# Optimization experiments

Measured on AMD Instinct MI355X. Metric: run time of the kernel, lower is better.

Reference implementation:

```python
import jax, jax.numpy as jnp
import numpy as np
import math

B, L, HID = 2, 2048, 1024
NH, DH = 16, 64
MASK_VAL = -1000000000.0  # half_precision_flag == False


def setup_inputs() -> dict:
    key = jax.random.key(0)
    ks = jax.random.split(key, 12)
    s = 0.02
    return {
        "queries": jax.random.normal(ks[0], (B, L, HID), jnp.float32),
        "keys": jax.random.normal(ks[1], (B, L, HID), jnp.float32),
        "values": jax.random.normal(ks[2], (B, L, HID), jnp.float32),
        "mask": jax.random.randint(ks[3], (B, L, L), 0, 2, jnp.int32),
        "Wq": jax.random.normal(ks[4], (HID, NH * DH), jnp.float32) * s,
        "bq": jnp.zeros((NH * DH,), jnp.float32),
        "Wk": jax.random.normal(ks[5], (HID, NH * DH), jnp.float32) * s,
        "bk": jnp.zeros((NH * DH,), jnp.float32),
        "Wv": jax.random.normal(ks[6], (HID, NH * DH), jnp.float32) * s,
        "bv": jnp.zeros((NH * DH,), jnp.float32),
        "Wo": jax.random.normal(ks[7], (NH * DH, HID), jnp.float32) * s,
        "bo": jnp.zeros((HID,), jnp.float32),
    }


def reference(queries, keys, values, mask, Wq, bq, Wk, bk, Wv, bv, Wo, bo):
    # Linear projections: (B, L, NH*DH)
    q = queries @ Wq + bq
    k = keys @ Wk + bk
    v = values @ Wv + bv
    # FAITHFUL to original: raw .view(B, NH, -1, DH) without transpose
    q = q.reshape(B, NH, L, DH)
    k = k.reshape(B, NH, L, DH)
    v = v.reshape(B, NH, L, DH)
    # scaled dot-product scores: (B, NH, L, L)
    scores = jnp.einsum("bhqd,bhkd->bhqk", q, k) / math.sqrt(DH)
    scores = jnp.where(mask[:, None, :, :] == 0, MASK_VAL, scores)
    probs = jax.nn.softmax(scores, axis=-1)  # dropout p=0 -> identity
    ctx = jnp.einsum("bhqk,bhkd->bhqd", probs, v)  # (B, NH, L, DH)
    # transpose(1,2) then flatten heads, as in original
    ctx = ctx.transpose(0, 2, 1, 3).reshape(B, L, NH * DH)
    return ctx @ Wo + bo
```

## Files before the change

kernel.cpp:

```cpp
#include <hip/hip_runtime.h>
#include <stdint.h>

typedef __bf16 bf16;
typedef __bf16 bf16x8 __attribute__((ext_vector_type(8)));
typedef __bf16 bf16x4 __attribute__((ext_vector_type(4)));
typedef float  f32x4  __attribute__((ext_vector_type(4)));
typedef short  s16x4  __attribute__((ext_vector_type(4)));
typedef unsigned long long ull;

#define GLOAD16(gptr, lptr)                                                     \
  __builtin_amdgcn_global_load_lds(                                             \
      (const __attribute__((address_space(1))) void*)(gptr),                    \
      (__attribute__((address_space(3))) void*)(lptr), 16, 0, 0)

#define MFMA16(a, b, c) __builtin_amdgcn_mfma_f32_16x16x32_bf16((a), (b), (c), 0, 0, 0)
#define MFMA16K16(a, b, c) __builtin_amdgcn_mfma_f32_16x16x16bf16_1k((a), (b), (c), 0, 0, 0)

static constexpr int B_ = 2, L_ = 2048, NH_ = 16, DH_ = 64;
static constexpr float QSCALE = 0.18033688011112042f;

__global__ __launch_bounds__(256) void k_prep(const float* __restrict__ q,
                                              const float* __restrict__ k,
                                              const float* __restrict__ v,
                                              const int* __restrict__ mask,
                                              const float* __restrict__ wq,
                                              const float* __restrict__ wk,
                                              const float* __restrict__ wv,
                                              const float* __restrict__ wo,
                                              bf16* __restrict__ X,
                                              bf16* __restrict__ Wt,
                                              ull* __restrict__ mb) {
  __shared__ float t[32][33];
  const int bid = blockIdx.x, tid = threadIdx.x;
  if (bid < 32768) {
    int tt = bid * 256 + tid;
    ull bal = __ballot(mask[tt] != 0);
    if ((tid & 63) == 0) mb[tt >> 6] = bal;
  } else if (bid < 45056) {
    int u = bid - 32768;
    int z = u >> 12, x = u & 4095;
    const float* in = z == 0 ? q : (z == 1 ? k : v);
    bf16* out = X + (size_t)z * 4194304;
    int i = x * 256 + tid;
    const float4 f = ((const float4*)in)[i];
    bf16x4 o = {(bf16)f.x, (bf16)f.y, (bf16)f.z, (bf16)f.w};
    ((bf16x4*)out)[i] = o;
  } else {
    int u = bid - 45056;
    int z = u >> 10, rem = u & 1023;
    const float* in = z == 0 ? wq : (z == 1 ? wk : (z == 2 ? wv : wo));
    bf16* out = Wt + (size_t)z * 1048576;
    int bx = (rem & 31) * 32, by = (rem >> 5) * 32;
    int x = tid & 31, y = tid >> 5;
#pragma unroll
    for (int r = 0; r < 4; ++r)
      t[y + r * 8][x] = in[(size_t)(by + y + r * 8) * 1024 + bx + x];
    __syncthreads();
#pragma unroll
    for (int r = 0; r < 4; ++r)
      out[(size_t)(bx + y + r * 8) * 1024 + by + x] = (bf16)t[x][y + r * 8];
  }
}

__global__ __launch_bounds__(256) void k_gemm3(const bf16* __restrict__ Xb,
                                               const bf16* __restrict__ Wb,
                                               const float* __restrict__ b0,
                                               const float* __restrict__ b1,
                                               const float* __restrict__ b2,
                                               bf16* __restrict__ Ob) {
  const int z = blockIdx.z;
  const bf16* A  = Xb + (size_t)z * 4194304;
  const bf16* Bt = Wb + (size_t)z * 1048576;
  const float* bias = z == 0 ? b0 : (z == 1 ? b1 : b2);
  bf16* C = Ob + (size_t)z * 4194304;
  const int m0 = blockIdx.y * 128, n0 = blockIdx.x * 128;
  __shared__ __align__(16) bf16 As[128 * 32];
  __shared__ __align__(16) bf16 Bs[128 * 32];
  const int tid = threadIdx.x, lane = tid & 63, w = tid >> 6, quad = lane >> 4, l15 = lane & 15;
  const int wm = (w & 1) * 64, wn = (w >> 1) * 64;
  f32x4 acc[4][4] = {};
  for (int kt = 0; kt < 32; ++kt) {
    const int kk = kt * 32;
#pragma unroll
    for (int i = 0; i < 2; ++i) {
      int s = tid + i * 256;
      int r = s >> 2, c = (s & 3) ^ ((r >> 1) & 3);
      GLOAD16(A + (size_t)(m0 + r) * 1024 + kk + c * 8, As + s * 8);
      GLOAD16(Bt + (size_t)(n0 + r) * 1024 + kk + c * 8, Bs + s * 8);
    }
    __syncthreads();
    bf16x8 af[4], bb[4];
#pragma unroll
    for (int i = 0; i < 4; ++i) {
      int ra = wm + i * 16 + l15, rb = wn + i * 16 + l15;
      af[i] = *(const bf16x8*)(As + (ra * 4 + (quad ^ ((ra >> 1) & 3))) * 8);
      bb[i] = *(const bf16x8*)(Bs + (rb * 4 + (quad ^ ((rb >> 1) & 3))) * 8);
    }
#pragma unroll
    for (int mi = 0; mi < 4; ++mi)
#pragma unroll
      for (int ni = 0; ni < 4; ++ni)
        acc[mi][ni] = MFMA16(af[mi], bb[ni], acc[mi][ni]);
    __syncthreads();
  }
  const float scale = (z == 0) ? QSCALE : 1.0f;
#pragma unroll
  for (int mi = 0; mi < 4; ++mi)
#pragma unroll
    for (int ni = 0; ni < 4; ++ni) {
      int row = m0 + wm + mi * 16 + quad * 4;
      int col = n0 + wn + ni * 16 + l15;
      float bz = bias[col];
      if (z == 2) {
        int b_ = row >> 11, l = row & 2047;
        int hh = l >> 7;
        int i0 = (l & 127) * 16 + (col >> 6);
        int d  = col & 63;
        bf16* dst = C + (size_t)(b_ * 16 + hh) * 131072;
#pragma unroll
        for (int r = 0; r < 4; ++r) {
          int iK = i0 + 16 * r;
          dst[((size_t)(iK >> 2) * 64 + d) * 4 + (iK & 3)] = (bf16)(acc[mi][ni][r] + bz);
        }
      } else {
#pragma unroll
        for (int r = 0; r < 4; ++r)
          C[(size_t)(row + r) * 1024 + col] = (bf16)((acc[mi][ni][r] + bz) * scale);
      }
    }
}

__global__ __launch_bounds__(256) void k_gemmo(const bf16* __restrict__ A,
                                               const bf16* __restrict__ Bt,
                                               const float* __restrict__ bias,
                                               float* __restrict__ C) {
  const int m0 = blockIdx.y * 64, n0 = blockIdx.x * 128;
  __shared__ __align__(16) bf16 As[64 * 32];
  __shared__ __align__(16) bf16 Bs[128 * 32];
  const int tid = threadIdx.x, lane = tid & 63, w = tid >> 6, quad = lane >> 4, l15 = lane & 15;
  const int wn = w * 32;
  f32x4 acc[4][2] = {};
  for (int kt = 0; kt < 32; ++kt) {
    const int kk = kt * 32;
    {
      int r = tid >> 2, c = (tid & 3) ^ ((r >> 1) & 3);
      GLOAD16(A + (size_t)(m0 + r) * 1024 + kk + c * 8, As + tid * 8);
    }
#pragma unroll
    for (int i = 0; i < 2; ++i) {
      int s = tid + i * 256;
      int r = s >> 2, c = (s & 3) ^ ((r >> 1) & 3);
      GLOAD16(Bt + (size_t)(n0 + r) * 1024 + kk + c * 8, Bs + s * 8);
    }
    __syncthreads();
    bf16x8 af[4], bb[2];
#pragma unroll
    for (int i = 0; i < 4; ++i) {
      int ra = i * 16 + l15;
      af[i] = *(const bf16x8*)(As + (ra * 4 + (quad ^ ((ra >> 1) & 3))) * 8);
    }
#pragma unroll
    for (int i = 0; i < 2; ++i) {
      int rb = wn + i * 16 + l15;
      bb[i] = *(const bf16x8*)(Bs + (rb * 4 + (quad ^ ((rb >> 1) & 3))) * 8);
    }
#pragma unroll
    for (int mi = 0; mi < 4; ++mi)
#pragma unroll
      for (int ni = 0; ni < 2; ++ni)
        acc[mi][ni] = MFMA16(af[mi], bb[ni], acc[mi][ni]);
    __syncthreads();
  }
#pragma unroll
  for (int mi = 0; mi < 4; ++mi)
#pragma unroll
    for (int ni = 0; ni < 2; ++ni) {
      int row = m0 + mi * 16 + quad * 4;
      int col = n0 + wn + ni * 16 + l15;
      float bz = bias[col];
#pragma unroll
      for (int r = 0; r < 4; ++r)
        C[(size_t)(row + r) * 1024 + col] = acc[mi][ni][r] + bz;
    }
}

__global__ __launch_bounds__(256) void k_flash(const bf16* __restrict__ Qp,
                                               const bf16* __restrict__ Kp,
                                               const bf16* __restrict__ Vtp,
                                               const ull* __restrict__ mb,
                                               bf16* __restrict__ ctx) {
  const int b = blockIdx.z, h = blockIdx.y, q0 = blockIdx.x * 128;
  const size_t HEAD = 131072;
  const bf16* Q  = Qp  + ((size_t)b * NH_ + h) * HEAD;
  const bf16* K  = Kp  + ((size_t)b * NH_ + h) * HEAD;
  const bf16* Vt = Vtp + ((size_t)b * NH_ + h) * HEAD;
  const ull* mrow = mb + (size_t)b * L_ * 32;

  __shared__ __align__(16) bf16 Ks[2][64 * 64];
  __shared__ __align__(16) bf16 Vs[2][64 * 64];
  __shared__ __align__(16) ull  Ms[2][256];

  const int tid = threadIdx.x, lane = tid & 63, w = tid >> 6, quad = lane >> 4, l15 = lane & 15;

  bf16x8 qf[2][2];
#pragma unroll
  for (int qb = 0; qb < 2; ++qb)
#pragma unroll
    for (int ks = 0; ks < 2; ++ks)
      qf[qb][ks] = *(const bf16x8*)(Q + (size_t)(q0 + w * 32 + qb * 16 + l15) * 64 + ks * 32 + quad * 8);

#pragma unroll
  for (int i = 0; i < 2; ++i) {
    int s = tid + i * 256;
    int key = s >> 3, c = (s & 7) ^ (key & 7);
    GLOAD16(K + (size_t)key * 64 + c * 8, Ks[0] + s * 8);
    GLOAD16(Vt + (size_t)s * 8, Vs[0] + s * 8);
  }
  if (w < 2) {
    int r = w * 64 + lane;
    GLOAD16(mrow + (size_t)(q0 + r) * 32, (bf16*)&Ms[0][0] + r * 8);
  }
  __syncthreads();

  f32x4 accO[2][4] = {};
  f32x4 accL[2] = {};
  const s16x4 onesf = {0x3F80, 0x3F80, 0x3F80, 0x3F80};

  for (int kt = 0; kt < 32; ++kt) {
    const int cur = kt & 1;
    if (kt + 1 < 32) {
      const int nxt = cur ^ 1;
#pragma unroll
      for (int i = 0; i < 2; ++i) {
        int s = tid + i * 256;
        int key = s >> 3, c = (s & 7) ^ (key & 7);
        GLOAD16(K + (size_t)((kt + 1) * 64 + key) * 64 + c * 8, Ks[nxt] + s * 8);
        GLOAD16(Vt + (size_t)(kt + 1) * 4096 + s * 8, Vs[nxt] + s * 8);
      }
      if ((kt & 1) && w < 2) {
        int r = w * 64 + lane;
        GLOAD16(mrow + (size_t)(q0 + r) * 32 + (kt + 1),
                (bf16*)&Ms[((kt + 1) >> 1) & 1][0] + r * 8);
      }
    }

    f32x4 st[4][2] = {};
#pragma unroll
    for (int ks = 0; ks < 2; ++ks)
#pragma unroll
      for (int kb = 0; kb < 4; ++kb) {
        int key = kb * 16 + l15;
        bf16x8 kf = *(const bf16x8*)(Ks[cur] + (key * 8 + ((ks * 4 + quad) ^ (key & 7))) * 8);
        st[kb][0] = MFMA16(kf, qf[0][ks], st[kb][0]);
        st[kb][1] = MFMA16(kf, qf[1][ks], st[kb][1]);
      }

    const ull* Mcur = Ms[(kt >> 1) & 1];
    const ull word0 = Mcur[(w * 32 + l15) * 2 + cur];
    const ull word1 = Mcur[(w * 32 + 16 + l15) * 2 + cur];
    s16x4 pf[4][2];
#pragma unroll
    for (int kb = 0; kb < 4; ++kb)
#pragma unroll
      for (int qb = 0; qb < 2; ++qb) {
        const unsigned nib = (unsigned)((qb ? word1 : word0) >> (kb * 16 + quad * 4)) & 0xFu;
        float p0 = (nib & 1u) ? __builtin_amdgcn_exp2f(st[kb][qb][0]) : 0.f;
        float p1 = (nib & 2u) ? __builtin_amdgcn_exp2f(st[kb][qb][1]) : 0.f;
        float p2 = (nib & 4u) ? __builtin_amdgcn_exp2f(st[kb][qb][2]) : 0.f;
        float p3 = (nib & 8u) ? __builtin_amdgcn_exp2f(st[kb][qb][3]) : 0.f;
        bf16x4 pb = {(bf16)p0, (bf16)p1, (bf16)p2, (bf16)p3};
        pf[kb][qb] = __builtin_bit_cast(s16x4, pb);
      }

#pragma unroll
    for (int kb = 0; kb < 4; ++kb) {
      accL[0] = MFMA16K16(pf[kb][0], onesf, accL[0]);
      accL[1] = MFMA16K16(pf[kb][1], onesf, accL[1]);
    }

#pragma unroll
    for (int kb = 0; kb < 4; ++kb)
#pragma unroll
      for (int db = 0; db < 4; ++db) {
        s16x4 vf = *(const s16x4*)(Vs[cur] + ((size_t)((kb * 4 + quad) * 64 + db * 16 + l15)) * 4);
        accO[0][db] = MFMA16K16(pf[kb][0], vf, accO[0][db]);
        accO[1][db] = MFMA16K16(pf[kb][1], vf, accO[1][db]);
      }
    __syncthreads();
  }

#pragma unroll
  for (int qb = 0; qb < 2; ++qb) {
    float rl[4];
#pragma unroll
    for (int r = 0; r < 4; ++r) rl[r] = 1.0f / accL[qb][r];
#pragma unroll
    for (int db = 0; db < 4; ++db) {
      const int col = h * 64 + db * 16 + l15;
#pragma unroll
      for (int r = 0; r < 4; ++r) {
        const int rowg = q0 + w * 32 + qb * 16 + quad * 4 + r;
        ctx[((size_t)b * L_ + rowg) * 1024 + col] = (bf16)(accO[qb][db][r] * rl[r]);
      }
    }
  }
}

extern "C" void kernel_launch(void* const* d_in, const int* in_sizes, int n_in,
                              void* d_out, int out_size, void* d_ws, size_t ws_size,
                              hipStream_t stream) {
  (void)in_sizes; (void)n_in; (void)out_size; (void)ws_size;
  const float* q    = (const float*)d_in[0];
  const float* k    = (const float*)d_in[1];
  const float* v    = (const float*)d_in[2];
  const int*   mask = (const int*)d_in[3];
  const float* Wq = (const float*)d_in[4];
  const float* bq = (const float*)d_in[5];
  const float* Wk = (const float*)d_in[6];
  const float* bk = (const float*)d_in[7];
  const float* Wv = (const float*)d_in[8];
  const float* bv = (const float*)d_in[9];
  const float* Wo = (const float*)d_in[10];
  const float* bo = (const float*)d_in[11];
  float* out = (float*)d_out;

  char* ws = (char*)d_ws;
  const size_t SX = (size_t)4096 * 1024 * 2;
  const size_t SW = (size_t)1024 * 1024 * 2;
  bf16* X   = (bf16*)(ws);
  bf16* Wt  = (bf16*)(ws + 3 * SX);
  bf16* QKV = (bf16*)(ws + 3 * SX + 4 * SW);
  bf16* Qp  = QKV;
  bf16* Kp  = QKV + 4194304;
  bf16* Vtp = QKV + 2 * 4194304;
  bf16* Ctx = (bf16*)(ws + 6 * SX + 4 * SW);
  ull* mbits = (ull*)(ws + 7 * SX + 4 * SW);

  dim3 blk(256);
  k_prep<<<49152, blk, 0, stream>>>(q, k, v, mask, Wq, Wk, Wv, Wo, X, Wt, mbits);

  k_gemm3<<<dim3(8, 32, 3), blk, 0, stream>>>(X, Wt, bq, bk, bv, QKV);

  k_flash<<<dim3(16, NH_, B_), blk, 0, stream>>>(Qp, Kp, Vtp, mbits, Ctx);

  k_gemmo<<<dim3(8, 64), blk, 0, stream>>>(Ctx, Wt + 3 * 1048576, bo, out);
}
```

Baseline: 273.9 us.

## Split attention key range across two blocks and merge partials in a combine kernel

The flash attention kernel now handles only half of the key tiles per block. The grid grows from 512 to 1024 blocks, which should raise occupancy across the CUs. Each half writes unnormalized fp32 partial outputs and row sums to workspace. A new combine kernel adds the two halves, normalizes them and writes the bf16 context. In exchange there is extra global memory traffic for the fp32 partials, one more kernel launch, and workspace aliasing over the dead X buffer and the region past the mask bits.

```diff
diff --git a/kernel.cpp b/kernel.cpp
--- a/kernel.cpp
+++ b/kernel.cpp
@@ -188,13 +188,21 @@
                                                const bf16* __restrict__ Kp,
                                                const bf16* __restrict__ Vtp,
                                                const ull* __restrict__ mb,
-                                               bf16* __restrict__ ctx) {
-  const int b = blockIdx.z, h = blockIdx.y, q0 = blockIdx.x * 128;
+                                               float* __restrict__ O0,
+                                               float* __restrict__ O1,
+                                               float* __restrict__ L0,
+                                               float* __restrict__ L1) {
+  const int b = blockIdx.z >> 1, half = blockIdx.z & 1;
+  const int h = blockIdx.y, q0 = blockIdx.x * 128;
+  const int kt0 = half * 16, ktend = kt0 + 16;
+  float* __restrict__ Op = half ? O1 : O0;
+  float* __restrict__ Lp = half ? L1 : L0;
   const size_t HEAD = 131072;
   const bf16* Q  = Qp  + ((size_t)b * NH_ + h) * HEAD;
   const bf16* K  = Kp  + ((size_t)b * NH_ + h) * HEAD;
   const bf16* Vt = Vtp + ((size_t)b * NH_ + h) * HEAD;
   const ull* mrow = mb + (size_t)b * L_ * 32;
+  const size_t obase = ((size_t)b * NH_ + h) * L_;
 
   __shared__ __align__(16) bf16 Ks[2][64 * 64];
   __shared__ __align__(16) bf16 Vs[2][64 * 64];
@@ -213,12 +221,12 @@
   for (int i = 0; i < 2; ++i) {
     int s = tid + i * 256;
     int key = s >> 3, c = (s & 7) ^ (key & 7);
-    GLOAD16(K + (size_t)key * 64 + c * 8, Ks[0] + s * 8);
-    GLOAD16(Vt + (size_t)s * 8, Vs[0] + s * 8);
+    GLOAD16(K + (size_t)(kt0 * 64 + key) * 64 + c * 8, Ks[0] + s * 8);
+    GLOAD16(Vt + (size_t)kt0 * 4096 + s * 8, Vs[0] + s * 8);
   }
   if (w < 2) {
     int r = w * 64 + lane;
-    GLOAD16(mrow + (size_t)(q0 + r) * 32, (bf16*)&Ms[0][0] + r * 8);
+    GLOAD16(mrow + (size_t)(q0 + r) * 32 + kt0, (bf16*)&Ms[0][0] + r * 8);
   }
   __syncthreads();
 
@@ -226,9 +234,9 @@
   f32x4 accL[2] = {};
   const s16x4 onesf = {0x3F80, 0x3F80, 0x3F80, 0x3F80};
 
-  for (int kt = 0; kt < 32; ++kt) {
+  for (int kt = kt0; kt < ktend; ++kt) {
     const int cur = kt & 1;
-    if (kt + 1 < 32) {
+    if (kt + 1 < ktend) {
       const int nxt = cur ^ 1;
 #pragma unroll
       for (int i = 0; i < 2; ++i) {
@@ -291,19 +299,42 @@
 
 #pragma unroll
   for (int qb = 0; qb < 2; ++qb) {
-    float rl[4];
-#pragma unroll
-    for (int r = 0; r < 4; ++r) rl[r] = 1.0f / accL[qb][r];
 #pragma unroll
     for (int db = 0; db < 4; ++db) {
-      const int col = h * 64 + db * 16 + l15;
+      const int d = db * 16 + l15;
 #pragma unroll
       for (int r = 0; r < 4; ++r) {
-        const int rowg = q0 + w * 32 + qb * 16 + quad * 4 + r;
-        ctx[((size_t)b * L_ + rowg) * 1024 + col] = (bf16)(accO[qb][db][r] * rl[r]);
-      }
-    }
-  }
+        const int qq = q0 + w * 32 + qb * 16 + quad * 4 + r;
+        Op[(obase + qq) * 64 + d] = accO[qb][db][r];
+      }
+    }
+    if (l15 == 0) {
+#pragma unroll
+      for (int r = 0; r < 4; ++r) {
+        const int qq = q0 + w * 32 + qb * 16 + quad * 4 + r;
+        Lp[obase + qq] = accL[qb][r];
+      }
+    }
+  }
+}
+
+__global__ __launch_bounds__(256) void k_comb(const float* __restrict__ O0,
+                                              const float* __restrict__ O1,
+                                              const float* __restrict__ L0,
+                                              const float* __restrict__ L1,
+                                              bf16* __restrict__ ctx) {
+  const int t = blockIdx.x * 256 + threadIdx.x;
+  const int d4 = t & 15;
+  const int q  = (t >> 4) & 2047;
+  const int bh = t >> 15;
+  const size_t base = (((size_t)bh * 2048 + q) * 64) + d4 * 4;
+  const float4 o0 = *(const float4*)(O0 + base);
+  const float4 o1 = *(const float4*)(O1 + base);
+  const float rl = 1.0f / (L0[(size_t)bh * 2048 + q] + L1[(size_t)bh * 2048 + q]);
+  const int b = bh >> 4, h = bh & 15;
+  bf16x4 r = {(bf16)((o0.x + o1.x) * rl), (bf16)((o0.y + o1.y) * rl),
+              (bf16)((o0.z + o1.z) * rl), (bf16)((o0.w + o1.w) * rl)};
+  *(bf16x4*)(ctx + ((size_t)(b * 2048 + q) * 1024 + h * 64 + d4 * 4)) = r;
 }
 
 extern "C" void kernel_launch(void* const* d_in, const int* in_sizes, int n_in,
@@ -327,6 +358,7 @@
   char* ws = (char*)d_ws;
   const size_t SX = (size_t)4096 * 1024 * 2;
   const size_t SW = (size_t)1024 * 1024 * 2;
+  const size_t MB1 = 1024 * 1024;
   bf16* X   = (bf16*)(ws);
   bf16* Wt  = (bf16*)(ws + 3 * SX);
   bf16* QKV = (bf16*)(ws + 3 * SX + 4 * SW);
@@ -335,13 +367,19 @@
   bf16* Vtp = QKV + 2 * 4194304;
   bf16* Ctx = (bf16*)(ws + 6 * SX + 4 * SW);
   ull* mbits = (ull*)(ws + 7 * SX + 4 * SW);
+  float* O0p = (float*)(ws);
+  float* L0p = (float*)(ws + 20 * MB1);
+  float* L1p = (float*)(ws + 21 * MB1);
+  float* O1p = (float*)(ws + 7 * SX + 4 * SW + MB1);
 
   dim3 blk(256);
   k_prep<<<49152, blk, 0, stream>>>(q, k, v, mask, Wq, Wk, Wv, Wo, X, Wt, mbits);
 
   k_gemm3<<<dim3(8, 32, 3), blk, 0, stream>>>(X, Wt, bq, bk, bv, QKV);
 
-  k_flash<<<dim3(16, NH_, B_), blk, 0, stream>>>(Qp, Kp, Vtp, mbits, Ctx);
+  k_flash<<<dim3(16, NH_, 2 * B_), blk, 0, stream>>>(Qp, Kp, Vtp, mbits,
+                                                     O0p, O1p, L0p, L1p);
+  k_comb<<<4096, blk, 0, stream>>>(O0p, O1p, L0p, L1p, Ctx);
 
   k_gemmo<<<dim3(8, 64), blk, 0, stream>>>(Ctx, Wt + 3 * 1048576, bo, out);
 }
```

Measured after the change: 279.4 us. +2.0%, slower.
